# Kernel tuning notes

Hardware: AMD Instinct MI355X
Metric: run time of the kernel (lower is better)

Reference implementation:

```python
import jax, jax.numpy as jnp
import numpy as np

GAMMA = 0.99
STEP_TYPE_LAST = 2  # alf.data_structures.StepType.LAST
T, B = 256, 65536


def setup_inputs() -> dict:
    key = jax.random.key(0)
    k = jax.random.split(key, 7)
    return {
        "reward": jax.random.normal(k[0], (T, B), dtype=jnp.float32),
        "discount": jax.random.uniform(k[1], (T, B), dtype=jnp.float32),
        "value": jax.random.normal(k[2], (T, B), dtype=jnp.float32),
        "target_value": jax.random.normal(k[3], (T, B), dtype=jnp.float32),
        "step_type": jax.random.randint(k[4], (T, B), 0, 3, dtype=jnp.int32),
        "rollout_b": jax.random.randint(k[5], (T, B), 0, 2, dtype=jnp.int32),
        "train_b": jax.random.randint(k[6], (T, B), 0, 2, dtype=jnp.int32),
    }


def _discounted_return(rewards, values, is_lasts, discounts):
    # Backward recursion:
    #   rets[T-1] = values[T-1]; acc[T-1] = values[T-1]
    #   rets[t] = acc[t+1] * discounts[t+1] + rewards[t+1]
    #   acc[t]  = is_lasts[t] * values[t] + (1 - is_lasts[t]) * rets[t]
    # returns rets[0:T-1]  (shape [T-1, B])
    il = is_lasts.astype(values.dtype)
    xs = (discounts[1:], rewards[1:], il[:-1], values[:-1])
    xs_rev = jax.tree_util.tree_map(lambda x: x[::-1], xs)  # scan t = T-2 .. 0

    def step(acc, x):
        d, r, l, v = x
        ret = acc * d + r
        acc_new = l * v + (1.0 - l) * ret
        return acc_new, ret

    _, rets_rev = jax.lax.scan(step, values[-1], xs_rev)
    return jax.lax.stop_gradient(rets_rev[::-1])  # [T-1, B]


def reference(reward, discount, value, target_value, step_type, rollout_b, train_b):
    discounts = discount * GAMMA
    b = (rollout_b != 0) | (train_b != 0)
    b = b.at[0].set(False)
    is_lasts = (step_type == STEP_TYPE_LAST) | b
    returns = _discounted_return(reward, target_value, is_lasts, discounts)
    v = value[:-1]
    loss = jnp.square(returns - v)                 # element_wise_squared_loss
    loss = jnp.concatenate([loss, jnp.zeros_like(loss[:1])], axis=0)  # extend zero -> [T, B]
    return loss
```

## Files before the change

### kernel.cpp

```cpp
#include <hip/hip_runtime.h>
#include <hip/hip_bf16.h>

#define T_STEPS 256
#define B_COLS  65536
#define GAMMA_F 0.99f


template <int N>
__device__ __forceinline__ float process_group(
    int i_hi, unsigned b, float acc,
    const float* __restrict__ reward,
    const float* __restrict__ discount,
    const float* __restrict__ value,
    const float* __restrict__ target_value,
    const int*   __restrict__ step_type,
    const int*   __restrict__ rollout_b,
    const int*   __restrict__ train_b,
    float*       __restrict__ out)
{
    float d[N], r[N], tv[N], v[N];
    int   st[N], rb[N], tb[N];

#pragma unroll
    for (int j = 0; j < N; ++j) {
        const unsigned idx  = (unsigned)(i_hi - j) * B_COLS + b;
        const unsigned idx1 = idx + B_COLS;
        d[j]  = discount[idx1];
        r[j]  = reward[idx1];
        tv[j] = target_value[idx];
        v[j]  = value[idx];
        st[j] = step_type[idx];
        rb[j] = rollout_b[idx];
        tb[j] = train_b[idx];
    }

#pragma unroll
    for (int j = 0; j < N; ++j) {
        const float ret  = fmaf(acc, d[j] * GAMMA_F, r[j]);
        const bool  l    = (st[j] == 2) | (rb[j] != 0) | (tb[j] != 0);
        acc = l ? tv[j] : ret;
        const float diff = ret - v[j];
        out[(unsigned)(i_hi - j) * B_COLS + b] = diff * diff;
    }
    return acc;
}

__global__ __launch_bounds__(256) void td_loss_kernel(
    const float* __restrict__ reward,
    const float* __restrict__ discount,
    const float* __restrict__ value,
    const float* __restrict__ target_value,
    const int*   __restrict__ step_type,
    const int*   __restrict__ rollout_b,
    const int*   __restrict__ train_b,
    float*       __restrict__ out)
{
    const unsigned b = blockIdx.x * blockDim.x + threadIdx.x;

    const unsigned last = (unsigned)(T_STEPS - 1) * B_COLS + b;
    float acc = target_value[last];
    out[last] = 0.0f;

    acc = process_group<6>(T_STEPS - 2, b, acc,
                           reward, discount, value, target_value,
                           step_type, rollout_b, train_b, out);

    for (int i = 248; i >= 8; i -= 8) {
        acc = process_group<8>(i, b, acc,
                               reward, discount, value, target_value,
                               step_type, rollout_b, train_b, out);
    }

    {
        const unsigned idx1 = B_COLS + b;
        const float d   = discount[idx1] * GAMMA_F;
        const float r   = reward[idx1];
        const float ret = fmaf(acc, d, r);
        const float v   = value[b];
        const float diff = ret - v;
        out[b] = diff * diff;
    }
}

extern "C" void kernel_launch(void* const* d_in, const int* in_sizes, int n_in,
                              void* d_out, int out_size, void* d_ws, size_t ws_size,
                              hipStream_t stream) {
    const float* reward       = (const float*)d_in[0];
    const float* discount     = (const float*)d_in[1];
    const float* value        = (const float*)d_in[2];
    const float* target_value = (const float*)d_in[3];
    const int*   step_type    = (const int*)d_in[4];
    const int*   rollout_b    = (const int*)d_in[5];
    const int*   train_b      = (const int*)d_in[6];
    float*       out          = (float*)d_out;

    const int block = 256;
    const int grid  = B_COLS / block;
    td_loss_kernel<<<grid, block, 0, stream>>>(
        reward, discount, value, target_value, step_type, rollout_b, train_b, out);
}
```

Measured before the change: 402.9 us.

## Parallelize the time recurrence with a chunked affine scan across threads

Replaces the fully serial per-column backward recurrence with a two-pass chunked scan. Each thread handles one 16-step chunk of one column and reduces its chunk to an affine map (alpha, beta). One thread per column then composes the chunk maps through shared memory to get each chunk's incoming accumulator, and all chunks then replay their steps in parallel to write the losses. This targets the old kernel's very low thread count, which left it latency bound. The costs are extra block synchronisation, a short serial pass, and narrower 32-column tiles that make each memory access segment smaller. The kernel also packs the three step-type/flag tests into a per-thread bitmask.

New measurement: 424.9 us. 5.4% more time.

```diff
diff --git a/kernel.cpp b/kernel.cpp
--- a/kernel.cpp
+++ b/kernel.cpp
@@ -1,14 +1,14 @@
 #include <hip/hip_runtime.h>
-#include <hip/hip_bf16.h>
 
 #define T_STEPS 256
-#define B_COLS  65536
+#define B_COLS  65536u
 #define GAMMA_F 0.99f
 
+#define CHUNK   16
+#define NCHUNK  (T_STEPS / CHUNK)
+#define BCOL    32
 
-template <int N>
-__device__ __forceinline__ float process_group(
-    int i_hi, unsigned b, float acc,
+__global__ __launch_bounds__(512, 4) void td_loss_kernel(
     const float* __restrict__ reward,
     const float* __restrict__ discount,
     const float* __restrict__ value,
@@ -18,67 +18,72 @@
     const int*   __restrict__ train_b,
     float*       __restrict__ out)
 {
-    float d[N], r[N], tv[N], v[N];
-    int   st[N], rb[N], tb[N];
+    const int x  = threadIdx.x;
+    const int ch = threadIdx.y;
+    const unsigned col  = blockIdx.x * BCOL + x;
+    const int      hi   = ch * CHUNK + (CHUNK - 1);
+    const unsigned base = (unsigned)hi * B_COLS + col;
 
+    __shared__ float s_alpha[NCHUNK][BCOL];
+    __shared__ float s_beta [NCHUNK][BCOL];
+    __shared__ float s_accin[NCHUNK][BCOL];
+
+    unsigned mask = 0;
 #pragma unroll
-    for (int j = 0; j < N; ++j) {
-        const unsigned idx  = (unsigned)(i_hi - j) * B_COLS + b;
-        const unsigned idx1 = idx + B_COLS;
-        d[j]  = discount[idx1];
+    for (int j = 0; j < CHUNK; ++j)
+        mask |= (unsigned)(step_type[base - (unsigned)j * B_COLS] == 2) << j;
+#pragma unroll
+    for (int j = 0; j < CHUNK; ++j)
+        mask |= (unsigned)(rollout_b[base - (unsigned)j * B_COLS] != 0) << j;
+#pragma unroll
+    for (int j = 0; j < CHUNK; ++j)
+        mask |= (unsigned)(train_b[base - (unsigned)j * B_COLS] != 0) << j;
+    if (ch == NCHUNK - 1) mask |= 1u;
+
+    float D[CHUNK], r[CHUNK], tv[CHUNK], v[CHUNK];
+#pragma unroll
+    for (int j = 0; j < CHUNK; ++j) {
+        const unsigned idx  = base - (unsigned)j * B_COLS;
+        const unsigned idx1 = (hi - j == T_STEPS - 1) ? idx : idx + B_COLS;
+        D[j]  = discount[idx1] * GAMMA_F;
         r[j]  = reward[idx1];
         tv[j] = target_value[idx];
         v[j]  = value[idx];
-        st[j] = step_type[idx];
-        rb[j] = rollout_b[idx];
-        tb[j] = train_b[idx];
     }
 
+    float alpha = 1.0f, beta = 0.0f;
 #pragma unroll
-    for (int j = 0; j < N; ++j) {
-        const float ret  = fmaf(acc, d[j] * GAMMA_F, r[j]);
-        const bool  l    = (st[j] == 2) | (rb[j] != 0) | (tb[j] != 0);
+    for (int j = 0; j < CHUNK; ++j) {
+        const bool  l = (mask >> j) & 1u;
+        const float g = l ? 0.0f : D[j];
+        const float o = l ? tv[j] : r[j];
+        beta  = fmaf(g, beta, o);
+        alpha *= g;
+    }
+    s_alpha[ch][x] = alpha;
+    s_beta [ch][x] = beta;
+    __syncthreads();
+
+    if (ch == 0) {
+        float acc = 0.0f;
+#pragma unroll
+        for (int k = NCHUNK - 1; k >= 0; --k) {
+            s_accin[k][x] = acc;
+            acc = fmaf(s_alpha[k][x], acc, s_beta[k][x]);
+        }
+    }
+    __syncthreads();
+
+    float acc = s_accin[ch][x];
+#pragma unroll
+    for (int j = 0; j < CHUNK; ++j) {
+        const float ret  = fmaf(acc, D[j], r[j]);
+        const bool  l    = (mask >> j) & 1u;
         acc = l ? tv[j] : ret;
         const float diff = ret - v[j];
-        out[(unsigned)(i_hi - j) * B_COLS + b] = diff * diff;
-    }
-    return acc;
-}
-
-__global__ __launch_bounds__(256) void td_loss_kernel(
-    const float* __restrict__ reward,
-    const float* __restrict__ discount,
-    const float* __restrict__ value,
-    const float* __restrict__ target_value,
-    const int*   __restrict__ step_type,
-    const int*   __restrict__ rollout_b,
-    const int*   __restrict__ train_b,
-    float*       __restrict__ out)
-{
-    const unsigned b = blockIdx.x * blockDim.x + threadIdx.x;
-
-    const unsigned last = (unsigned)(T_STEPS - 1) * B_COLS + b;
-    float acc = target_value[last];
-    out[last] = 0.0f;
-
-    acc = process_group<6>(T_STEPS - 2, b, acc,
-                           reward, discount, value, target_value,
-                           step_type, rollout_b, train_b, out);
-
-    for (int i = 248; i >= 8; i -= 8) {
-        acc = process_group<8>(i, b, acc,
-                               reward, discount, value, target_value,
-                               step_type, rollout_b, train_b, out);
-    }
-
-    {
-        const unsigned idx1 = B_COLS + b;
-        const float d   = discount[idx1] * GAMMA_F;
-        const float r   = reward[idx1];
-        const float ret = fmaf(acc, d, r);
-        const float v   = value[b];
-        const float diff = ret - v;
-        out[b] = diff * diff;
+        float o = diff * diff;
+        if (hi - j == T_STEPS - 1) o = 0.0f;
+        out[base - (unsigned)j * B_COLS] = o;
     }
 }
 
@@ -94,8 +99,8 @@
     const int*   train_b      = (const int*)d_in[6];
     float*       out          = (float*)d_out;
 
-    const int block = 256;
-    const int grid  = B_COLS / block;
+    dim3 block(BCOL, NCHUNK);
+    dim3 grid(B_COLS / BCOL);
     td_loss_kernel<<<grid, block, 0, stream>>>(
         reward, discount, value, target_value, step_type, rollout_b, train_b, out);
 }
```
